# Optimization experiments

Measured on AMD Instinct MI355X. Metric: run time of the kernel, lower is better.

## Reference

```python
import jax, jax.numpy as jnp
import numpy as np
from jax import lax

IMG = 28
K = 3
OUT = IMG - K + 1  # 26

def setup_inputs() -> dict:
    key = jax.random.key(0)
    k1, k2, k3 = jax.random.split(key, 3)
    B = 32768
    x = jax.random.normal(k1, (B, IMG * IMG), dtype=jnp.float32)
    conv_w = jax.random.normal(k2, (K, K), dtype=jnp.float32)
    W = jax.random.normal(k3, (IMG * IMG - 0, 1), dtype=jnp.float32)  # placeholder
    W = jax.random.normal(k3, (OUT * OUT, 10), dtype=jnp.float32) * 0.02
    b = jnp.zeros((10,), dtype=jnp.float32)
    return {"x": x, "conv_w": conv_w, "W": W, "b": b}

def reference(x, conv_w, W, b):
    B = x.shape[0]
    img = x.reshape(B, 1, IMG, IMG)            # NCHW
    ker = conv_w.reshape(1, 1, K, K)           # OIHW
    # The original Convolve is cross-correlation (slice * weight), which
    # matches lax.conv_general_dilated's default semantics.
    conv = lax.conv_general_dilated(
        img, ker, window_strides=(1, 1), padding='VALID',
        dimension_numbers=('NCHW', 'OIHW', 'NCHW'))  # [B,1,26,26]
    h = jax.nn.relu(conv.reshape(B, OUT * OUT))
    return h @ W + b
```

## Files before the change

kernel.cpp:

```cpp
#include <hip/hip_runtime.h>

#define IMGD 28
#define OUTD 26
#define NCLS 10
#define NIMG 64
#define BROWS 8
#define BUNITS 56
#define BWORDS (NIMG * BROWS * IMGD)
#define THREADS 1024
#define LDSTRIDE 11

typedef float v2f __attribute__((ext_vector_type(2)));

__device__ __forceinline__ void gload_lds16(const float* gp, float* lp) {
    __builtin_amdgcn_global_load_lds(
        (const __attribute__((address_space(1))) void*)gp,
        (__attribute__((address_space(3))) void*)lp, 16, 0, 0);
}

__device__ __forceinline__ void stage_band(const float* __restrict__ x,
                                           int img_base, int B, int r0,
                                           float* buf, int wv, int lane)
{
#pragma unroll
    for (int it = 0; it < 4; ++it) {
        const int fw = it * 16 + wv;
        if (fw < 56) {
            const int f = fw * 64 + lane;
            const int g = f / 56;
            const int s = f - g * 56;
            const int q = s ^ (g & 7);
            int gi = img_base + g; if (gi >= B) gi = B - 1;
            const float* gp = x + (size_t)gi * (IMGD * IMGD) + r0 * IMGD + q * 4;
            gload_lds16(gp, buf + fw * 256);
        }
    }
}

template<int WID, int NU, int OFF>
__device__ __forceinline__ void strip_compute(
    const float* buf, int lane, int u_col, int li, int nout,
    int wrow0, int c0, const float (&kk)[9],
    const float* __restrict__ Wp, v2f* acc)
{
    const float4* b4 = (const float4*)buf;
    const int sw = lane & 7;
    float R[5][4 * NU];
#pragma unroll
    for (int i = 0; i < 5; ++i) {
        if (i < nout + 2) {
            const int u = (li + i) * 7 + u_col;
            float4 a = b4[lane * 56 + (u ^ sw)];
            R[i][0] = a.x; R[i][1] = a.y; R[i][2] = a.z; R[i][3] = a.w;
            if (NU == 2) {
                float4 c = b4[lane * 56 + ((u + 1) ^ sw)];
                R[i][4] = c.x; R[i][5] = c.y; R[i][6] = c.z; R[i][7] = c.w;
            }
        }
    }
#pragma unroll
    for (int o = 0; o < 3; ++o) {
        if (o < nout) {
            const float *X = R[o], *Y = R[o + 1], *Z = R[o + 2];
#pragma unroll
            for (int c = 0; c < WID; ++c) {
                float p0 = fmaf(X[OFF+c], kk[0], X[OFF+c+1] * kk[1]);
                p0 = fmaf(X[OFF+c+2], kk[2], p0);
                float p1 = fmaf(Y[OFF+c], kk[3], Y[OFF+c+1] * kk[4]);
                p1 = fmaf(Y[OFF+c+2], kk[5], p1);
                float p2 = fmaf(Z[OFF+c], kk[6], Z[OFF+c+1] * kk[7]);
                p2 = fmaf(Z[OFF+c+2], kk[8], p2);
                float v = fmaxf((p0 + p1) + p2, 0.0f);
                const float* wr = Wp + ((size_t)(wrow0 + o) * OUTD + (c0 + c)) * NCLS;
#pragma unroll
                for (int p = 0; p < 5; ++p) {
                    v2f wvv = *(const v2f*)(wr + 2 * p);
                    v2f vv; vv[0] = v; vv[1] = v;
                    acc[p] += vv * wvv;
                }
            }
        }
    }
}

__global__ __launch_bounds__(THREADS) void fused_conv_relu_fc(
    const float* __restrict__ x,
    const float* __restrict__ cw,
    const float* __restrict__ Wp,
    const float* __restrict__ bp,
    float* __restrict__ out,
    int B)
{
    __shared__ float lds[2 * BWORDS];

    const int lane = threadIdx.x & 63;
    const int wv   = __builtin_amdgcn_readfirstlane((int)(threadIdx.x >> 6));
    const int rg   = wv >> 3;
    const int cs   = wv & 7;
    const int img_base = blockIdx.x * NIMG;

    float kk[9];
#pragma unroll
    for (int i = 0; i < 9; ++i) kk[i] = cw[i];

    v2f acc[5];
#pragma unroll
    for (int p = 0; p < 5; ++p) { acc[p][0] = 0.0f; acc[p][1] = 0.0f; }

    stage_band(x, img_base, B, 0, lds, wv, lane);
    asm volatile("s_waitcnt vmcnt(0)" ::: "memory");
    __syncthreads();

    for (int b = 0; b < 5; ++b) {
        if (b < 4) {
            const int r0n = (b + 1 < 4) ? 6 * (b + 1) : 20;
            stage_band(x, img_base, B, r0n, lds + ((b + 1) & 1) * BWORDS, wv, lane);
        }
        const float* buf = lds + (b & 1) * BWORDS;
        int nout, li, wrow0;
        if (b < 4) { nout = 3; li = rg * 3; wrow0 = 6 * b + rg * 3; }
        else       { nout = (rg == 0) ? 2 : 0; li = 4; wrow0 = 24; }
        if (nout) {
            if      (cs < 5)  strip_compute<4,2,0>(buf, lane, cs, li, nout, wrow0, 4*cs, kk, Wp, acc);
            else if (cs == 5) strip_compute<2,1,0>(buf, lane, 5,  li, nout, wrow0, 20,   kk, Wp, acc);
            else if (cs == 6) strip_compute<2,2,2>(buf, lane, 5,  li, nout, wrow0, 22,   kk, Wp, acc);
            else              strip_compute<2,1,0>(buf, lane, 6,  li, nout, wrow0, 24,   kk, Wp, acc);
        }
        asm volatile("s_waitcnt vmcnt(0)" ::: "memory");
        __syncthreads();
    }

    float* part = lds;
    float* myp = &part[(wv * 64 + lane) * LDSTRIDE];
#pragma unroll
    for (int p = 0; p < 5; ++p) { myp[2*p] = acc[p][0]; myp[2*p+1] = acc[p][1]; }
    __syncthreads();

    const int o = threadIdx.x;
    if (o < NIMG * NCLS) {
        const int im = o / NCLS;
        const int c  = o - im * NCLS;
        float s = bp[c];
#pragma unroll
        for (int w2 = 0; w2 < 16; ++w2)
            s += part[(w2 * 64 + im) * LDSTRIDE + c];
        if (img_base + im < B)
            out[(size_t)(img_base + im) * NCLS + c] = s;
    }
}

extern "C" void kernel_launch(void* const* d_in, const int* in_sizes, int n_in,
                              void* d_out, int out_size, void* d_ws, size_t ws_size,
                              hipStream_t stream) {
    const float* x  = (const float*)d_in[0];
    const float* cw = (const float*)d_in[1];
    const float* Wp = (const float*)d_in[2];
    const float* bp = (const float*)d_in[3];
    float* out = (float*)d_out;

    const int B = in_sizes[0] / (IMGD * IMGD);
    const int grid = (B + NIMG - 1) / NIMG;

    fused_conv_relu_fc<<<grid, THREADS, 0, stream>>>(x, cw, Wp, bp, out, B);
}
```

Measured before the change: 37.83 us.

## Stage 4-row bands with halo carried in registers and deeper prefetch

Stages the input in seven non-overlapping 4-row bands instead of five overlapping 8-row bands. The second row-group of waves keeps the last two rows of each band in registers so the halo is not reloaded. The swizzle is replaced by a 29-unit padded row stride. Loads are issued two bands ahead with per-wave partial vmcnt waits and raw s_barrier instead of waiting on all loads every step. This is meant to cut redundant global traffic and load-wait stalls, at the cost of more barriers and fragile vmcnt accounting. The two row groups also become unbalanced, since one of them is idle on the first band.

New measurement: 32.55 us. 14.0% less time.

```diff
diff --git a/kernel.cpp b/kernel.cpp
--- a/kernel.cpp
+++ b/kernel.cpp
@@ -4,9 +4,9 @@
 #define OUTD 26
 #define NCLS 10
 #define NIMG 64
-#define BROWS 8
-#define BUNITS 56
-#define BWORDS (NIMG * BROWS * IMGD)
+#define UPB 29
+#define BWORDS (NIMG * UPB * 4)
+#define NBAND 7
 #define THREADS 1024
 #define LDSTRIDE 11
 
@@ -23,13 +23,13 @@
                                            float* buf, int wv, int lane)
 {
 #pragma unroll
-    for (int it = 0; it < 4; ++it) {
+    for (int it = 0; it < 2; ++it) {
         const int fw = it * 16 + wv;
-        if (fw < 56) {
+        if (fw < UPB) {
             const int f = fw * 64 + lane;
-            const int g = f / 56;
-            const int s = f - g * 56;
-            const int q = s ^ (g & 7);
+            const int g = f / UPB;
+            const int s = f - g * UPB;
+            const int q = (s == 28) ? 27 : s;
             int gi = img_base + g; if (gi >= B) gi = B - 1;
             const float* gp = x + (size_t)gi * (IMGD * IMGD) + r0 * IMGD + q * 4;
             gload_lds16(gp, buf + fw * 256);
@@ -37,53 +37,102 @@
     }
 }
 
-template<int WID, int NU, int OFF>
-__device__ __forceinline__ void strip_compute(
-    const float* buf, int lane, int u_col, int li, int nout,
-    int wrow0, int c0, const float (&kk)[9],
-    const float* __restrict__ Wp, v2f* acc)
+template<int NU>
+__device__ __forceinline__ void read_row(const float* buf, int lane, int br, int u0,
+                                         float* dst)
 {
     const float4* b4 = (const float4*)buf;
-    const int sw = lane & 7;
-    float R[5][4 * NU];
 #pragma unroll
-    for (int i = 0; i < 5; ++i) {
-        if (i < nout + 2) {
-            const int u = (li + i) * 7 + u_col;
-            float4 a = b4[lane * 56 + (u ^ sw)];
-            R[i][0] = a.x; R[i][1] = a.y; R[i][2] = a.z; R[i][3] = a.w;
-            if (NU == 2) {
-                float4 c = b4[lane * 56 + ((u + 1) ^ sw)];
-                R[i][4] = c.x; R[i][5] = c.y; R[i][6] = c.z; R[i][7] = c.w;
-            }
-        }
+    for (int u = 0; u < NU; ++u) {
+        float4 a = b4[lane * UPB + br * 7 + u0 + u];
+        dst[4*u+0] = a.x; dst[4*u+1] = a.y; dst[4*u+2] = a.z; dst[4*u+3] = a.w;
     }
+}
+
+template<int WID, int OFF>
+__device__ __forceinline__ void conv_row(const float* X, const float* Y, const float* Z,
+                                         const float (&kk)[9],
+                                         const float* __restrict__ wr, v2f* acc)
+{
 #pragma unroll
-    for (int o = 0; o < 3; ++o) {
-        if (o < nout) {
-            const float *X = R[o], *Y = R[o + 1], *Z = R[o + 2];
+    for (int c = 0; c < WID; ++c) {
+        float p0 = fmaf(X[OFF+c], kk[0], X[OFF+c+1] * kk[1]);
+        p0 = fmaf(X[OFF+c+2], kk[2], p0);
+        float p1 = fmaf(Y[OFF+c], kk[3], Y[OFF+c+1] * kk[4]);
+        p1 = fmaf(Y[OFF+c+2], kk[5], p1);
+        float p2 = fmaf(Z[OFF+c], kk[6], Z[OFF+c+1] * kk[7]);
+        p2 = fmaf(Z[OFF+c+2], kk[8], p2);
+        float v = fmaxf((p0 + p1) + p2, 0.0f);
+        const float* w = wr + c * NCLS;
 #pragma unroll
-            for (int c = 0; c < WID; ++c) {
-                float p0 = fmaf(X[OFF+c], kk[0], X[OFF+c+1] * kk[1]);
-                p0 = fmaf(X[OFF+c+2], kk[2], p0);
-                float p1 = fmaf(Y[OFF+c], kk[3], Y[OFF+c+1] * kk[4]);
-                p1 = fmaf(Y[OFF+c+2], kk[5], p1);
-                float p2 = fmaf(Z[OFF+c], kk[6], Z[OFF+c+1] * kk[7]);
-                p2 = fmaf(Z[OFF+c+2], kk[8], p2);
-                float v = fmaxf((p0 + p1) + p2, 0.0f);
-                const float* wr = Wp + ((size_t)(wrow0 + o) * OUTD + (c0 + c)) * NCLS;
-#pragma unroll
-                for (int p = 0; p < 5; ++p) {
-                    v2f wvv = *(const v2f*)(wr + 2 * p);
-                    v2f vv; vv[0] = v; vv[1] = v;
-                    acc[p] += vv * wvv;
-                }
-            }
+        for (int p = 0; p < 5; ++p) {
+            v2f wv2 = *(const v2f*)(w + 2 * p);
+            v2f vv; vv[0] = v; vv[1] = v;
+            acc[p] += vv * wv2;
         }
     }
 }
 
-__global__ __launch_bounds__(THREADS) void fused_conv_relu_fc(
+template<int WID, int NU, int OFF>
+__device__ __forceinline__ void run_all(
+    const float* __restrict__ x, int img_base, int B,
+    float* lds0, int wv, int lane, int rg, int u0, int c0,
+    const float* __restrict__ cw, const float* __restrict__ Wp, v2f* acc)
+{
+    float kk[9];
+#pragma unroll
+    for (int i = 0; i < 9; ++i) kk[i] = cw[i];
+
+    float S[2][4 * NU];
+
+    stage_band(x, img_base, B, 0, lds0,          wv, lane);
+    stage_band(x, img_base, B, 4, lds0 + BWORDS, wv, lane);
+
+    for (int k = 0; k < NBAND; ++k) {
+        if (k < NBAND - 1) {
+            if (wv < 13) asm volatile("s_waitcnt vmcnt(2)" ::: "memory");
+            else         asm volatile("s_waitcnt vmcnt(1)" ::: "memory");
+        } else {
+            asm volatile("s_waitcnt vmcnt(0)" ::: "memory");
+        }
+        __builtin_amdgcn_s_barrier();
+
+        const float* buf = lds0 + (k & 1) * BWORDS;
+
+        if (rg == 0) {
+            float R[4][4 * NU];
+#pragma unroll
+            for (int br = 0; br < 4; ++br) read_row<NU>(buf, lane, br, u0, R[br]);
+            conv_row<WID, OFF>(R[0], R[1], R[2], kk,
+                               Wp + ((size_t)(4 * k) * OUTD + c0) * NCLS, acc);
+            conv_row<WID, OFF>(R[1], R[2], R[3], kk,
+                               Wp + ((size_t)(4 * k + 1) * OUTD + c0) * NCLS, acc);
+        } else {
+            if (k > 0) {
+                float T[2][4 * NU];
+                read_row<NU>(buf, lane, 0, u0, T[0]);
+                read_row<NU>(buf, lane, 1, u0, T[1]);
+                conv_row<WID, OFF>(S[0], S[1], T[0], kk,
+                                   Wp + ((size_t)(4 * k - 2) * OUTD + c0) * NCLS, acc);
+                conv_row<WID, OFF>(S[1], T[0], T[1], kk,
+                                   Wp + ((size_t)(4 * k - 1) * OUTD + c0) * NCLS, acc);
+            }
+            if (k < NBAND - 1) {
+                read_row<NU>(buf, lane, 2, u0, S[0]);
+                read_row<NU>(buf, lane, 3, u0, S[1]);
+            }
+        }
+
+        asm volatile("" ::: "memory");
+        __builtin_amdgcn_s_barrier();
+        asm volatile("" ::: "memory");
+
+        if (k + 2 < NBAND)
+            stage_band(x, img_base, B, 4 * (k + 2), lds0 + (k & 1) * BWORDS, wv, lane);
+    }
+}
+
+__global__ __launch_bounds__(THREADS, 8) void fused_conv_relu_fc(
     const float* __restrict__ x,
     const float* __restrict__ cw,
     const float* __restrict__ Wp,
@@ -99,36 +148,16 @@
     const int cs   = wv & 7;
     const int img_base = blockIdx.x * NIMG;
 
-    float kk[9];
-#pragma unroll
-    for (int i = 0; i < 9; ++i) kk[i] = cw[i];
-
     v2f acc[5];
 #pragma unroll
     for (int p = 0; p < 5; ++p) { acc[p][0] = 0.0f; acc[p][1] = 0.0f; }
 
-    stage_band(x, img_base, B, 0, lds, wv, lane);
-    asm volatile("s_waitcnt vmcnt(0)" ::: "memory");
+    if      (cs < 5)  run_all<4,2,0>(x, img_base, B, lds, wv, lane, rg, cs, 4*cs, cw, Wp, acc);
+    else if (cs == 5) run_all<2,1,0>(x, img_base, B, lds, wv, lane, rg, 5,  20,   cw, Wp, acc);
+    else if (cs == 6) run_all<2,2,2>(x, img_base, B, lds, wv, lane, rg, 5,  22,   cw, Wp, acc);
+    else              run_all<2,1,0>(x, img_base, B, lds, wv, lane, rg, 6,  24,   cw, Wp, acc);
+
     __syncthreads();
-
-    for (int b = 0; b < 5; ++b) {
-        if (b < 4) {
-            const int r0n = (b + 1 < 4) ? 6 * (b + 1) : 20;
-            stage_band(x, img_base, B, r0n, lds + ((b + 1) & 1) * BWORDS, wv, lane);
-        }
-        const float* buf = lds + (b & 1) * BWORDS;
-        int nout, li, wrow0;
-        if (b < 4) { nout = 3; li = rg * 3; wrow0 = 6 * b + rg * 3; }
-        else       { nout = (rg == 0) ? 2 : 0; li = 4; wrow0 = 24; }
-        if (nout) {
-            if      (cs < 5)  strip_compute<4,2,0>(buf, lane, cs, li, nout, wrow0, 4*cs, kk, Wp, acc);
-            else if (cs == 5) strip_compute<2,1,0>(buf, lane, 5,  li, nout, wrow0, 20,   kk, Wp, acc);
-            else if (cs == 6) strip_compute<2,2,2>(buf, lane, 5,  li, nout, wrow0, 22,   kk, Wp, acc);
-            else              strip_compute<2,1,0>(buf, lane, 6,  li, nout, wrow0, 24,   kk, Wp, acc);
-        }
-        asm volatile("s_waitcnt vmcnt(0)" ::: "memory");
-        __syncthreads();
-    }
 
     float* part = lds;
     float* myp = &part[(wv * 64 + lane) * LDSTRIDE];
```

## Split images into two row-halves per block, stage input as fp16 in LDS

Applied to the files above, without the earlier changes.

Each block now handles 15 input rows (13 output rows) of 64 images instead of the full image, with two blocks per image group combining results via atomicAdd into a zeroed output. The input is loaded through registers and converted to fp16 before being stored in LDS, halving LDS footprint and allowing more resident blocks. Each wave computes a 13-row column strip with rolling row registers. This adds a memset launch, atomics and fp16 rounding of inputs, which may affect accuracy.

Measured after the change: 38.38 us. Within noise of the previous version (+1.4%).

```diff
diff --git a/kernel.cpp b/kernel.cpp
--- a/kernel.cpp
+++ b/kernel.cpp
@@ -4,86 +4,93 @@
 #define OUTD 26
 #define NCLS 10
 #define NIMG 64
-#define BROWS 8
-#define BUNITS 56
-#define BWORDS (NIMG * BROWS * IMGD)
-#define THREADS 1024
+#define SLAB 15
+#define SLABF4 105
+#define TOTF4 (NIMG * SLABF4)
+#define RPADH 32
+#define IMGU 61
+#define THREADS 512
 #define LDSTRIDE 11
 
 typedef float v2f __attribute__((ext_vector_type(2)));
 
-__device__ __forceinline__ void gload_lds16(const float* gp, float* lp) {
-    __builtin_amdgcn_global_load_lds(
-        (const __attribute__((address_space(1))) void*)gp,
-        (__attribute__((address_space(3))) void*)lp, 16, 0, 0);
+template<int WID, int NRD, int OFF>
+__device__ __forceinline__ void read_rowh(const unsigned short* ldsh, int lane,
+                                          int r4, int U0, float* R)
+{
+    const uint4* b4 = (const uint4*)ldsh;
+    const int base = lane * IMGU + r4 + U0;
+    unsigned int w[4 * NRD];
+    uint4 a = b4[base];
+    w[0] = a.x; w[1] = a.y; w[2] = a.z; w[3] = a.w;
+    if constexpr (NRD == 2) {
+        uint4 b = b4[base + 1];
+        w[4] = b.x; w[5] = b.y; w[6] = b.z; w[7] = b.w;
+    }
+#pragma unroll
+    for (int i = 0; i < WID + 2; ++i) {
+        const int hh = OFF + i;
+        unsigned int word = w[hh >> 1];
+        unsigned short u = (hh & 1) ? (unsigned short)(word >> 16)
+                                    : (unsigned short)(word & 0xffffu);
+        R[i] = (float)__builtin_bit_cast(_Float16, u);
+    }
 }
 
-__device__ __forceinline__ void stage_band(const float* __restrict__ x,
-                                           int img_base, int B, int r0,
-                                           float* buf, int wv, int lane)
+template<int WID>
+__device__ __forceinline__ void conv_row(const float* X, const float* Y, const float* Z,
+                                         const float (&kk)[9],
+                                         const float* __restrict__ wr, v2f* acc)
 {
 #pragma unroll
-    for (int it = 0; it < 4; ++it) {
-        const int fw = it * 16 + wv;
-        if (fw < 56) {
-            const int f = fw * 64 + lane;
-            const int g = f / 56;
-            const int s = f - g * 56;
-            const int q = s ^ (g & 7);
-            int gi = img_base + g; if (gi >= B) gi = B - 1;
-            const float* gp = x + (size_t)gi * (IMGD * IMGD) + r0 * IMGD + q * 4;
-            gload_lds16(gp, buf + fw * 256);
+    for (int c = 0; c < WID; ++c) {
+        float p0 = fmaf(X[c], kk[0], X[c+1] * kk[1]);
+        p0 = fmaf(X[c+2], kk[2], p0);
+        float p1 = fmaf(Y[c], kk[3], Y[c+1] * kk[4]);
+        p1 = fmaf(Y[c+2], kk[5], p1);
+        float p2 = fmaf(Z[c], kk[6], Z[c+1] * kk[7]);
+        p2 = fmaf(Z[c+2], kk[8], p2);
+        float v = fmaxf((p0 + p1) + p2, 0.0f);
+        const float* w = wr + c * NCLS;
+#pragma unroll
+        for (int p = 0; p < 5; ++p) {
+            v2f wv2 = *(const v2f*)(w + 2 * p);
+            v2f vv; vv[0] = v; vv[1] = v;
+            acc[p] += vv * wv2;
         }
     }
 }
 
-template<int WID, int NU, int OFF>
-__device__ __forceinline__ void strip_compute(
-    const float* buf, int lane, int u_col, int li, int nout,
-    int wrow0, int c0, const float (&kk)[9],
-    const float* __restrict__ Wp, v2f* acc)
+template<int WID, int NRD, int OFF>
+__device__ __forceinline__ void strip13(const unsigned short* ldsh, int lane,
+                                        int U0, int c0, int wrow0,
+                                        const float (&kk)[9],
+                                        const float* __restrict__ Wp, v2f* acc)
 {
-    const float4* b4 = (const float4*)buf;
-    const int sw = lane & 7;
-    float R[5][4 * NU];
-#pragma unroll
-    for (int i = 0; i < 5; ++i) {
-        if (i < nout + 2) {
-            const int u = (li + i) * 7 + u_col;
-            float4 a = b4[lane * 56 + (u ^ sw)];
-            R[i][0] = a.x; R[i][1] = a.y; R[i][2] = a.z; R[i][3] = a.w;
-            if (NU == 2) {
-                float4 c = b4[lane * 56 + ((u + 1) ^ sw)];
-                R[i][4] = c.x; R[i][5] = c.y; R[i][6] = c.z; R[i][7] = c.w;
-            }
-        }
-    }
-#pragma unroll
-    for (int o = 0; o < 3; ++o) {
-        if (o < nout) {
-            const float *X = R[o], *Y = R[o + 1], *Z = R[o + 2];
-#pragma unroll
-            for (int c = 0; c < WID; ++c) {
-                float p0 = fmaf(X[OFF+c], kk[0], X[OFF+c+1] * kk[1]);
-                p0 = fmaf(X[OFF+c+2], kk[2], p0);
-                float p1 = fmaf(Y[OFF+c], kk[3], Y[OFF+c+1] * kk[4]);
-                p1 = fmaf(Y[OFF+c+2], kk[5], p1);
-                float p2 = fmaf(Z[OFF+c], kk[6], Z[OFF+c+1] * kk[7]);
-                p2 = fmaf(Z[OFF+c+2], kk[8], p2);
-                float v = fmaxf((p0 + p1) + p2, 0.0f);
-                const float* wr = Wp + ((size_t)(wrow0 + o) * OUTD + (c0 + c)) * NCLS;
-#pragma unroll
-                for (int p = 0; p < 5; ++p) {
-                    v2f wvv = *(const v2f*)(wr + 2 * p);
-                    v2f vv; vv[0] = v; vv[1] = v;
-                    acc[p] += vv * wvv;
-                }
-            }
-        }
-    }
+    float A[WID+2], Bv[WID+2], C[WID+2];
+    read_rowh<WID,NRD,OFF>(ldsh, lane, 0, U0, A);
+    read_rowh<WID,NRD,OFF>(ldsh, lane, 4, U0, Bv);
+#define OUTR(j, X, Y, Z, rin)                                            \
+    read_rowh<WID,NRD,OFF>(ldsh, lane, 4*(rin), U0, Z);                  \
+    conv_row<WID>(X, Y, Z, kk,                                           \
+                  Wp + ((size_t)(wrow0 + (j)) * OUTD + c0) * NCLS, acc);
+    OUTR(0,  A,  Bv, C,  2)
+    OUTR(1,  Bv, C,  A,  3)
+    OUTR(2,  C,  A,  Bv, 4)
+    OUTR(3,  A,  Bv, C,  5)
+    OUTR(4,  Bv, C,  A,  6)
+    OUTR(5,  C,  A,  Bv, 7)
+    OUTR(6,  A,  Bv, C,  8)
+    OUTR(7,  Bv, C,  A,  9)
+    OUTR(8,  C,  A,  Bv, 10)
+    OUTR(9,  A,  Bv, C,  11)
+    OUTR(10, Bv, C,  A,  12)
+    OUTR(11, C,  A,  Bv, 13)
+    OUTR(12, A,  Bv, C,  14)
+#undef OUTR
 }
 
-__global__ __launch_bounds__(THREADS) void fused_conv_relu_fc(
+__global__ __launch_bounds__(THREADS, 4) void fused_conv_relu_fc(
     const float* __restrict__ x,
     const float* __restrict__ cw,
     const float* __restrict__ Wp,
@@ -91,13 +98,42 @@
     float* __restrict__ out,
     int B)
 {
-    __shared__ float lds[2 * BWORDS];
+    __shared__ __align__(16) unsigned short ldsh[NIMG * IMGU * 8];
 
-    const int lane = threadIdx.x & 63;
-    const int wv   = __builtin_amdgcn_readfirstlane((int)(threadIdx.x >> 6));
-    const int rg   = wv >> 3;
-    const int cs   = wv & 7;
-    const int img_base = blockIdx.x * NIMG;
+    const int t    = threadIdx.x;
+    const int lane = t & 63;
+    const int wv   = __builtin_amdgcn_readfirstlane((int)(t >> 6));
+    const int grp  = blockIdx.x >> 1;
+    const int h    = blockIdx.x & 1;
+    const int img_base = grp * NIMG;
+    const int r0 = h * 13;
+
+    float4 v[14];
+#pragma unroll
+    for (int it = 0; it < 14; ++it) {
+        int F = it * THREADS + t; if (F >= TOTF4) F = TOTF4 - 1;
+        int g = F / SLABF4;
+        int s = F - g * SLABF4;
+        int gi = img_base + g; if (gi >= B) gi = B - 1;
+        v[it] = *(const float4*)(x + (size_t)gi * (IMGD*IMGD) + r0 * IMGD + s * 4);
+    }
+#pragma unroll
+    for (int it = 0; it < 14; ++it) {
+        int F0 = it * THREADS + t;
+        int F = F0 >= TOTF4 ? TOTF4 - 1 : F0;
+        int g = F / SLABF4;
+        int s = F - g * SLABF4;
+        int r = s / 7;
+        int c4 = s - r * 7;
+        ushort4 o;
+        o.x = __builtin_bit_cast(unsigned short, (_Float16)v[it].x);
+        o.y = __builtin_bit_cast(unsigned short, (_Float16)v[it].y);
+        o.z = __builtin_bit_cast(unsigned short, (_Float16)v[it].z);
+        o.w = __builtin_bit_cast(unsigned short, (_Float16)v[it].w);
+        if (F0 < TOTF4)
+            *(ushort4*)&ldsh[g * (IMGU * 8) + r * RPADH + c4 * 4] = o;
+    }
+    __syncthreads();
 
     float kk[9];
 #pragma unroll
@@ -107,45 +143,31 @@
 #pragma unroll
     for (int p = 0; p < 5; ++p) { acc[p][0] = 0.0f; acc[p][1] = 0.0f; }
 
-    stage_band(x, img_base, B, 0, lds, wv, lane);
-    asm volatile("s_waitcnt vmcnt(0)" ::: "memory");
+    if      (wv == 0) strip13<4,1,0>(ldsh, lane, 0, 0,  r0, kk, Wp, acc);
+    else if (wv == 1) strip13<4,2,4>(ldsh, lane, 0, 4,  r0, kk, Wp, acc);
+    else if (wv == 2) strip13<4,1,0>(ldsh, lane, 1, 8,  r0, kk, Wp, acc);
+    else if (wv == 3) strip13<4,2,4>(ldsh, lane, 1, 12, r0, kk, Wp, acc);
+    else if (wv == 4) strip13<4,1,0>(ldsh, lane, 2, 16, r0, kk, Wp, acc);
+    else if (wv == 5) strip13<4,2,4>(ldsh, lane, 2, 20, r0, kk, Wp, acc);
+    else if (wv == 6) strip13<2,1,0>(ldsh, lane, 3, 24, r0, kk, Wp, acc);
+
     __syncthreads();
 
-    for (int b = 0; b < 5; ++b) {
-        if (b < 4) {
-            const int r0n = (b + 1 < 4) ? 6 * (b + 1) : 20;
-            stage_band(x, img_base, B, r0n, lds + ((b + 1) & 1) * BWORDS, wv, lane);
-        }
-        const float* buf = lds + (b & 1) * BWORDS;
-        int nout, li, wrow0;
-        if (b < 4) { nout = 3; li = rg * 3; wrow0 = 6 * b + rg * 3; }
-        else       { nout = (rg == 0) ? 2 : 0; li = 4; wrow0 = 24; }
-        if (nout) {
-            if      (cs < 5)  strip_compute<4,2,0>(buf, lane, cs, li, nout, wrow0, 4*cs, kk, Wp, acc);
-            else if (cs == 5) strip_compute<2,1,0>(buf, lane, 5,  li, nout, wrow0, 20,   kk, Wp, acc);
-            else if (cs == 6) strip_compute<2,2,2>(buf, lane, 5,  li, nout, wrow0, 22,   kk, Wp, acc);
-            else              strip_compute<2,1,0>(buf, lane, 6,  li, nout, wrow0, 24,   kk, Wp, acc);
-        }
-        asm volatile("s_waitcnt vmcnt(0)" ::: "memory");
-        __syncthreads();
-    }
-
-    float* part = lds;
+    float* part = (float*)ldsh;
     float* myp = &part[(wv * 64 + lane) * LDSTRIDE];
 #pragma unroll
     for (int p = 0; p < 5; ++p) { myp[2*p] = acc[p][0]; myp[2*p+1] = acc[p][1]; }
     __syncthreads();
 
-    const int o = threadIdx.x;
-    if (o < NIMG * NCLS) {
+    for (int o = t; o < NIMG * NCLS; o += THREADS) {
         const int im = o / NCLS;
         const int c  = o - im * NCLS;
-        float s = bp[c];
+        float s = (h == 0) ? bp[c] : 0.0f;
 #pragma unroll
-        for (int w2 = 0; w2 < 16; ++w2)
+        for (int w2 = 0; w2 < 8; ++w2)
             s += part[(w2 * 64 + im) * LDSTRIDE + c];
         if (img_base + im < B)
-            out[(size_t)(img_base + im) * NCLS + c] = s;
+            atomicAdd(&out[(size_t)(img_base + im) * NCLS + c], s);
     }
 }
 
@@ -159,7 +181,8 @@
     float* out = (float*)d_out;
 
     const int B = in_sizes[0] / (IMGD * IMGD);
-    const int grid = (B + NIMG - 1) / NIMG;
+    const int ngrp = (B + NIMG - 1) / NIMG;
 
-    fused_conv_relu_fc<<<grid, THREADS, 0, stream>>>(x, cw, Wp, bp, out, B);
+    hipMemsetAsync(d_out, 0, (size_t)out_size * sizeof(float), stream);
+    fused_conv_relu_fc<<<ngrp * 2, THREADS, 0, stream>>>(x, cw, Wp, bp, out, B);
 }
```
